# Kernel optimization log

Hardware: AMD Instinct MI355X
Metric: run time of the kernel (lower is better)

## Reference

```python
import jax, jax.numpy as jnp
import numpy as np

EPS = 1e-08


def setup_inputs() -> dict:
    key = jax.random.key(0)
    k_x, k_w1, k_b1, k_w2, k_b2 = jax.random.split(key, 5)
    B, C, T = 64, 64, 4000
    x = jax.random.normal(k_x, (B, C, T, 1), dtype=jnp.float32)
    # 1x1 Conv2D with in_channels=1, out_channels=8 -> weight is an 8-vector + bias
    w1 = jax.random.normal(k_w1, (8,), dtype=jnp.float32) * 0.5
    b1 = jax.random.normal(k_b1, (8,), dtype=jnp.float32) * 0.1
    w2 = jax.random.normal(k_w2, (8,), dtype=jnp.float32) * 0.5
    b2 = jax.random.normal(k_b2, (8,), dtype=jnp.float32) * 0.1
    # gamma is initialized to 0 in the module (residual identity at init);
    # use a nonzero value so the attention path is exercised numerically.
    gamma = jnp.float32(0.5)
    return {"x": x, "w1": w1, "b1": b1, "w2": w2, "b2": b2, "gamma": gamma}


def reference(x, w1, b1, w2, b2, gamma):
    B, C, T, _ = x.shape  # (B, num_ch, T, 1)
    # 1x1 conv with C_in=1: broadcast multiply-add, then flatten (T, 8) -> T*8
    q = (x * w1 + b1).reshape(B, C, T * 8)  # proj_query (B, C, T*8)
    k = (x * w2 + b2).reshape(B, C, T * 8)  # proj_key   (B, C, T*8)
    # energy = Q @ K^T  -> (B, C, C)
    energy = jnp.einsum('bcd,bed->bce', q, k)
    # custom min-max normalization along last axis, then softmax
    max_h = jnp.max(energy, axis=2, keepdims=True)
    min_h = jnp.min(energy, axis=2, keepdims=True)
    energy = (energy - min_h) / (max_h - min_h + EPS)
    attention = jax.nn.softmax(energy, axis=-1)
    xs = x[..., 0]  # squeeze last dim -> (B, C, T)
    # attention^T @ xs  (transpose_a=True)
    attended = jnp.einsum('bec,bet->bct', attention, xs)
    return gamma * attended[..., None] + x
```

## Files before the change

kernel.cpp:

```cpp
#include <hip/hip_runtime.h>

#define BB 64
#define CC 64
#define TT 4000

#define SLABS 16
#define TSLAB 250
#define GP_PITCH 264

#define TPB 128
#define NT2 ((TT + TPB - 1) / TPB)
#define XPITCH 132
#define APITCH 72

#define GPART_ELEMS ((size_t)SLABS * BB * CC * CC)
#define SPART_ELEMS ((size_t)SLABS * BB * CC)

typedef short short8 __attribute__((ext_vector_type(8)));
typedef float f32x16 __attribute__((ext_vector_type(16)));

__device__ __forceinline__ short f2bf(float f) {
    unsigned u = __float_as_uint(f);
    u = (u + 0x7FFFu + ((u >> 16) & 1u)) >> 16;
    return (short)u;
}
__device__ __forceinline__ float bfpair(unsigned u) {
    return __uint_as_float(u << 16) + __uint_as_float(u & 0xFFFF0000u);
}

__global__ __launch_bounds__(256)
void gram_mfma(const float* __restrict__ x, float* __restrict__ G_part,
               float* __restrict__ S_part) {
    __shared__ short xs[CC * GP_PITCH];
    __shared__ float sred[4 * 64];
    const int b    = blockIdx.x / SLABS;
    const int slab = blockIdx.x % SLABS;
    const int t0   = slab * TSLAB;
    const int tid  = threadIdx.x;
    const int lane = tid & 63;
    const int wave = tid >> 6;
    const float* xb = x + (size_t)b * CC * TT;

    for (int i = tid; i < 64 * 64; i += 256) {
        int row = i >> 6, tq = i & 63;
        float4 v = make_float4(0.f, 0.f, 0.f, 0.f);
        if (tq < 62) {
            v = *(const float4*)(xb + row * TT + t0 + 4 * tq);
        } else if (tq == 62) {
            const float* p = xb + row * TT + t0 + 248;
            v.x = p[0]; v.y = p[1];
        }
        short4 sv;
        sv.x = f2bf(v.x); sv.y = f2bf(v.y); sv.z = f2bf(v.z); sv.w = f2bf(v.w);
        int pc = (tq >> 1) ^ (row & 7);
        *(short4*)(xs + row * GP_PITCH + pc * 8 + (tq & 1) * 4) = sv;
    }
    __syncthreads();

    {
        const short* rowp = xs + lane * GP_PITCH;
        float s = 0.f;
        #pragma unroll
        for (int j = 0; j < 8; ++j) {
            int pc = (wave * 8 + j) ^ (lane & 7);
            uint2 u0 = *(const uint2*)(rowp + pc * 8);
            uint2 u1 = *(const uint2*)(rowp + pc * 8 + 4);
            s += bfpair(u0.x) + bfpair(u0.y) + bfpair(u1.x) + bfpair(u1.y);
        }
        sred[wave * 64 + lane] = s;
    }
    __syncthreads();
    if (tid < 64) {
        float s = sred[tid] + sred[64 + tid] + sred[128 + tid] + sred[192 + tid];
        S_part[(slab * BB + b) * CC + tid] = s;
    }

    const int r0 = (wave >> 1) * 32, c0 = (wave & 1) * 32;
    const int m = lane & 31, half = lane >> 5;
    f32x16 acc;
    #pragma unroll
    for (int z = 0; z < 16; ++z) acc[z] = 0.f;
    #pragma unroll
    for (int ks = 0; ks < 16; ++ks) {
        const int ck = ks * 2 + half;
        short8 av = *(const short8*)(xs + (r0 + m) * GP_PITCH + (ck ^ (m & 7)) * 8);
        short8 bv = *(const short8*)(xs + (c0 + m) * GP_PITCH + (ck ^ (m & 7)) * 8);
        acc = __builtin_amdgcn_mfma_f32_32x32x16_bf16(av, bv, acc, 0, 0, 0);
    }
    float* gp = G_part + ((size_t)slab * BB + b) * (CC * CC);
    #pragma unroll
    for (int r = 0; r < 16; ++r) {
        const int row = (r & 3) + 8 * (r >> 2) + 4 * half;
        gp[(r0 + row) * CC + (c0 + m)] = acc[r];
    }
}

__global__ __launch_bounds__(256)
void softmax_fused(const float* __restrict__ w1, const float* __restrict__ b1,
                   const float* __restrict__ w2, const float* __restrict__ b2,
                   const float* __restrict__ G_part, const float* __restrict__ S_part,
                   float* __restrict__ attG) {
    __shared__ float Es[64 * 65];
    __shared__ float Sb[64];
    __shared__ float red_mn[4 * 64], red_mx[4 * 64], red_sm[4 * 64];
    const int b   = blockIdx.x;
    const int tid = threadIdx.x;
    const int c = tid & 63, q = tid >> 6;

    for (int j = tid; j < 4096; j += 256) {
        float s = 0.f;
        #pragma unroll
        for (int sl = 0; sl < SLABS; ++sl)
            s += G_part[((size_t)sl * BB + b) * 4096 + j];
        Es[(j >> 6) * 65 + (j & 63)] = s;
    }
    if (tid < 64) {
        float s = 0.f;
        #pragma unroll
        for (int sl = 0; sl < SLABS; ++sl)
            s += S_part[(sl * BB + b) * CC + tid];
        Sb[tid] = s;
    }
    float A = 0.f, Bc = 0.f, Be = 0.f, Cc = 0.f;
    #pragma unroll
    for (int j = 0; j < 8; ++j) {
        float a1 = w1[j], a2 = w2[j], q1 = b1[j], q2 = b2[j];
        A += a1 * a2; Bc += a1 * q2; Be += q1 * a2; Cc += q1 * q2;
    }
    Cc *= (float)TT;
    __syncthreads();

    const float sc = Sb[c];
    float ev[16], mn = 1e30f, mx = -1e30f;
    #pragma unroll
    for (int i = 0; i < 16; ++i) {
        const int e = 16 * q + i;
        float en = A * Es[c * 65 + e] + Bc * sc + Be * Sb[e] + Cc;
        ev[i] = en;
        mn = fminf(mn, en); mx = fmaxf(mx, en);
    }
    red_mn[q * 64 + c] = mn; red_mx[q * 64 + c] = mx;
    __syncthreads();
    mn = fminf(fminf(red_mn[c], red_mn[64 + c]), fminf(red_mn[128 + c], red_mn[192 + c]));
    mx = fmaxf(fmaxf(red_mx[c], red_mx[64 + c]), fmaxf(red_mx[128 + c], red_mx[192 + c]));
    const float ninv = 1.f / (mx - mn + 1e-8f);
    float pv[16], ls = 0.f;
    #pragma unroll
    for (int i = 0; i < 16; ++i) {
        float p = __expf((ev[i] - mn) * ninv);
        pv[i] = p; ls += p;
    }
    red_sm[q * 64 + c] = ls;
    __syncthreads();
    const float rinv = 1.f / (red_sm[c] + red_sm[64 + c] + red_sm[128 + c] + red_sm[192 + c]);
    #pragma unroll
    for (int i = 0; i < 16; ++i) Es[c * 65 + 16 * q + i] = pv[i] * rinv;
    __syncthreads();
    float* ab = attG + (size_t)b * 4096;
    for (int j = tid; j < 4096; j += 256) {
        int cc = j >> 6, ee = j & 63;
        ab[j] = Es[ee * 65 + cc];
    }
}

__global__ __launch_bounds__(256)
void apply_mfma(const float* __restrict__ x, const float* __restrict__ attG,
                const float* __restrict__ gamma, float* __restrict__ out) {
    __shared__ float xs[CC * XPITCH];
    __shared__ short al[CC * APITCH];
    const int b  = blockIdx.x / NT2;
    const int t0 = (blockIdx.x % NT2) * TPB;
    const int tid = threadIdx.x;
    const int lane = tid & 63, wave = tid >> 6;
    const float* xb = x + (size_t)b * CC * TT;
    const float* ab = attG + (size_t)b * CC * CC;

    for (int i = tid; i < CC * (TPB / 4); i += 256) {
        int e = i >> 5, p = i & 31;
        int t = t0 + 4 * p;
        float4 v = make_float4(0.f, 0.f, 0.f, 0.f);
        if (t < TT) v = *(const float4*)(xb + e * TT + t);
        *(float4*)(xs + e * XPITCH + 4 * p) = v;
    }
    for (int i = tid; i < CC * CC / 4; i += 256) {
        int c = i >> 4, qq = i & 15;
        float4 v = *(const float4*)(ab + c * CC + 4 * qq);
        short4 sv;
        sv.x = f2bf(v.x); sv.y = f2bf(v.y); sv.z = f2bf(v.z); sv.w = f2bf(v.w);
        *(short4*)(al + c * APITCH + 4 * qq) = sv;
    }
    __syncthreads();

    const int m = lane & 31, half = lane >> 5;
    const int c0 = (wave & 1) * 32;
    const int tb = (wave >> 1) * 64;
    f32x16 acc0, acc1;
    #pragma unroll
    for (int z = 0; z < 16; ++z) { acc0[z] = 0.f; acc1[z] = 0.f; }

    #pragma unroll
    for (int ks = 0; ks < 4; ++ks) {
        short8 av = *(const short8*)(al + (c0 + m) * APITCH + ks * 16 + 8 * half);
        const int eb = ks * 16 + 8 * half;
        short8 bv0, bv1;
        #pragma unroll
        for (int j = 0; j < 8; ++j) {
            bv0[j] = f2bf(xs[(eb + j) * XPITCH + tb + m]);
            bv1[j] = f2bf(xs[(eb + j) * XPITCH + tb + 32 + m]);
        }
        acc0 = __builtin_amdgcn_mfma_f32_32x32x16_bf16(av, bv0, acc0, 0, 0, 0);
        acc1 = __builtin_amdgcn_mfma_f32_32x32x16_bf16(av, bv1, acc1, 0, 0, 0);
    }

    const float gm = gamma[0];
    float* ob = out + (size_t)b * CC * TT;
    #pragma unroll
    for (int r = 0; r < 16; ++r) {
        const int row = (r & 3) + 8 * (r >> 2) + 4 * half;
        const int c = c0 + row;
        const int tl0 = tb + m, tl1 = tb + 32 + m;
        const int tg0 = t0 + tl0, tg1 = t0 + tl1;
        if (tg0 < TT) ob[c * TT + tg0] = gm * acc0[r] + xs[c * XPITCH + tl0];
        if (tg1 < TT) ob[c * TT + tg1] = gm * acc1[r] + xs[c * XPITCH + tl1];
    }
}

extern "C" void kernel_launch(void* const* d_in, const int* in_sizes, int n_in,
                              void* d_out, int out_size, void* d_ws, size_t ws_size,
                              hipStream_t stream) {
    const float* x  = (const float*)d_in[0];
    const float* w1 = (const float*)d_in[1];
    const float* b1 = (const float*)d_in[2];
    const float* w2 = (const float*)d_in[3];
    const float* b2 = (const float*)d_in[4];
    const float* gm = (const float*)d_in[5];
    float* out = (float*)d_out;

    float* G_part = (float*)d_ws;
    float* S_part = G_part + GPART_ELEMS;
    float* attG   = S_part + SPART_ELEMS;

    hipLaunchKernelGGL(gram_mfma, dim3(BB * SLABS), dim3(256), 0, stream,
                       x, G_part, S_part);
    hipLaunchKernelGGL(softmax_fused, dim3(BB), dim3(256), 0, stream,
                       w1, b1, w2, b2, G_part, S_part, attG);
    hipLaunchKernelGGL(apply_mfma, dim3(BB * NT2), dim3(256), 0, stream,
                       x, attG, gm, out);
}
```

Before: 166.4 us.

## Halve gram slabs, batch loads, and pass attention as bf16 to apply kernel

The gram kernel now processes two 250-step chunks per block with 8 slabs instead of 16. This halves the partial Gram matrices written to and re-read from the workspace, and loads are batched eight float4s at a time for more memory-level parallelism. The softmax kernel reduces partials with float4 loads and writes the attention matrix directly as packed bf16, so the apply kernel loads it with wide short8 reads instead of converting per block. The trade-off is fewer gram blocks (512) and an extra barrier per chunk, which may reduce parallelism.

```diff
diff --git a/kernel.cpp b/kernel.cpp
--- a/kernel.cpp
+++ b/kernel.cpp
@@ -4,8 +4,9 @@
 #define CC 64
 #define TT 4000
 
-#define SLABS 16
+#define SLABS 8
 #define TSLAB 250
+#define SLABT (2 * TSLAB)
 #define GP_PITCH 264
 
 #define TPB 128
@@ -35,58 +36,78 @@
     __shared__ float sred[4 * 64];
     const int b    = blockIdx.x / SLABS;
     const int slab = blockIdx.x % SLABS;
-    const int t0   = slab * TSLAB;
     const int tid  = threadIdx.x;
     const int lane = tid & 63;
     const int wave = tid >> 6;
     const float* xb = x + (size_t)b * CC * TT;
 
-    for (int i = tid; i < 64 * 64; i += 256) {
-        int row = i >> 6, tq = i & 63;
-        float4 v = make_float4(0.f, 0.f, 0.f, 0.f);
-        if (tq < 62) {
-            v = *(const float4*)(xb + row * TT + t0 + 4 * tq);
-        } else if (tq == 62) {
-            const float* p = xb + row * TT + t0 + 248;
-            v.x = p[0]; v.y = p[1];
-        }
-        short4 sv;
-        sv.x = f2bf(v.x); sv.y = f2bf(v.y); sv.z = f2bf(v.z); sv.w = f2bf(v.w);
-        int pc = (tq >> 1) ^ (row & 7);
-        *(short4*)(xs + row * GP_PITCH + pc * 8 + (tq & 1) * 4) = sv;
-    }
-    __syncthreads();
-
-    {
-        const short* rowp = xs + lane * GP_PITCH;
-        float s = 0.f;
-        #pragma unroll
-        for (int j = 0; j < 8; ++j) {
-            int pc = (wave * 8 + j) ^ (lane & 7);
-            uint2 u0 = *(const uint2*)(rowp + pc * 8);
-            uint2 u1 = *(const uint2*)(rowp + pc * 8 + 4);
-            s += bfpair(u0.x) + bfpair(u0.y) + bfpair(u1.x) + bfpair(u1.y);
-        }
-        sred[wave * 64 + lane] = s;
-    }
+    const int r0 = (wave >> 1) * 32, c0 = (wave & 1) * 32;
+    const int m = lane & 31, half = lane >> 5;
+    f32x16 acc;
+    #pragma unroll
+    for (int z = 0; z < 16; ++z) acc[z] = 0.f;
+    float s_acc = 0.f;
+
+    for (int ch = 0; ch < 2; ++ch) {
+        const int t0 = slab * SLABT + ch * TSLAB;
+
+        #pragma unroll
+        for (int g = 0; g < 2; ++g) {
+            float4 v[8];
+            #pragma unroll
+            for (int k = 0; k < 8; ++k) {
+                const int i = tid + 256 * (g * 8 + k);
+                const int row = i >> 6, tq = i & 63;
+                float4 w = make_float4(0.f, 0.f, 0.f, 0.f);
+                if (tq < 62) {
+                    w = *(const float4*)(xb + row * TT + t0 + 4 * tq);
+                } else if (tq == 62) {
+                    const float* p = xb + row * TT + t0 + 248;
+                    w.x = p[0]; w.y = p[1];
+                }
+                v[k] = w;
+            }
+            #pragma unroll
+            for (int k = 0; k < 8; ++k) {
+                const int i = tid + 256 * (g * 8 + k);
+                const int row = i >> 6, tq = i & 63;
+                short4 sv;
+                sv.x = f2bf(v[k].x); sv.y = f2bf(v[k].y);
+                sv.z = f2bf(v[k].z); sv.w = f2bf(v[k].w);
+                const int pc = (tq >> 1) ^ (row & 7);
+                *(short4*)(xs + row * GP_PITCH + pc * 8 + (tq & 1) * 4) = sv;
+            }
+        }
+        __syncthreads();
+
+        {
+            const short* rowp = xs + lane * GP_PITCH;
+            #pragma unroll
+            for (int j = 0; j < 8; ++j) {
+                const int pc = (wave * 8 + j) ^ (lane & 7);
+                uint2 u0 = *(const uint2*)(rowp + pc * 8);
+                uint2 u1 = *(const uint2*)(rowp + pc * 8 + 4);
+                s_acc += bfpair(u0.x) + bfpair(u0.y) + bfpair(u1.x) + bfpair(u1.y);
+            }
+        }
+
+        #pragma unroll
+        for (int ks = 0; ks < 16; ++ks) {
+            const int ck = ks * 2 + half;
+            short8 av = *(const short8*)(xs + (r0 + m) * GP_PITCH + (ck ^ (m & 7)) * 8);
+            short8 bv = *(const short8*)(xs + (c0 + m) * GP_PITCH + (ck ^ (m & 7)) * 8);
+            acc = __builtin_amdgcn_mfma_f32_32x32x16_bf16(av, bv, acc, 0, 0, 0);
+        }
+        __syncthreads();
+    }
+
+    sred[wave * 64 + lane] = s_acc;
     __syncthreads();
     if (tid < 64) {
         float s = sred[tid] + sred[64 + tid] + sred[128 + tid] + sred[192 + tid];
         S_part[(slab * BB + b) * CC + tid] = s;
     }
 
-    const int r0 = (wave >> 1) * 32, c0 = (wave & 1) * 32;
-    const int m = lane & 31, half = lane >> 5;
-    f32x16 acc;
-    #pragma unroll
-    for (int z = 0; z < 16; ++z) acc[z] = 0.f;
-    #pragma unroll
-    for (int ks = 0; ks < 16; ++ks) {
-        const int ck = ks * 2 + half;
-        short8 av = *(const short8*)(xs + (r0 + m) * GP_PITCH + (ck ^ (m & 7)) * 8);
-        short8 bv = *(const short8*)(xs + (c0 + m) * GP_PITCH + (ck ^ (m & 7)) * 8);
-        acc = __builtin_amdgcn_mfma_f32_32x32x16_bf16(av, bv, acc, 0, 0, 0);
-    }
     float* gp = G_part + ((size_t)slab * BB + b) * (CC * CC);
     #pragma unroll
     for (int r = 0; r < 16; ++r) {
@@ -99,7 +120,7 @@
 void softmax_fused(const float* __restrict__ w1, const float* __restrict__ b1,
                    const float* __restrict__ w2, const float* __restrict__ b2,
                    const float* __restrict__ G_part, const float* __restrict__ S_part,
-                   float* __restrict__ attG) {
+                   unsigned short* __restrict__ attB) {
     __shared__ float Es[64 * 65];
     __shared__ float Sb[64];
     __shared__ float red_mn[4 * 64], red_mx[4 * 64], red_sm[4 * 64];
@@ -107,12 +128,18 @@
     const int tid = threadIdx.x;
     const int c = tid & 63, q = tid >> 6;
 
-    for (int j = tid; j < 4096; j += 256) {
-        float s = 0.f;
-        #pragma unroll
-        for (int sl = 0; sl < SLABS; ++sl)
-            s += G_part[((size_t)sl * BB + b) * 4096 + j];
-        Es[(j >> 6) * 65 + (j & 63)] = s;
+    #pragma unroll
+    for (int j4 = 0; j4 < 4; ++j4) {
+        const int jj = tid + 256 * j4;
+        float4 s = make_float4(0.f, 0.f, 0.f, 0.f);
+        #pragma unroll
+        for (int sl = 0; sl < SLABS; ++sl) {
+            const float4 g = *(const float4*)(G_part + ((size_t)sl * BB + b) * 4096 + 4 * jj);
+            s.x += g.x; s.y += g.y; s.z += g.z; s.w += g.w;
+        }
+        const int row = jj >> 4, col = (jj & 15) * 4;
+        float* e = Es + row * 65 + col;
+        e[0] = s.x; e[1] = s.y; e[2] = s.z; e[3] = s.w;
     }
     if (tid < 64) {
         float s = 0.f;
@@ -156,15 +183,18 @@
     #pragma unroll
     for (int i = 0; i < 16; ++i) Es[c * 65 + 16 * q + i] = pv[i] * rinv;
     __syncthreads();
-    float* ab = attG + (size_t)b * 4096;
-    for (int j = tid; j < 4096; j += 256) {
-        int cc = j >> 6, ee = j & 63;
-        ab[j] = Es[ee * 65 + cc];
+    unsigned short* ab = attB + (size_t)b * 4096;
+    #pragma unroll
+    for (int j2 = tid; j2 < 2048; j2 += 256) {
+        const int cc = j2 >> 5, e0 = (j2 & 31) * 2;
+        const unsigned lo = (unsigned short)f2bf(Es[e0 * 65 + cc]);
+        const unsigned hi = (unsigned short)f2bf(Es[(e0 + 1) * 65 + cc]);
+        *(unsigned*)(ab + cc * 64 + e0) = lo | (hi << 16);
     }
 }
 
 __global__ __launch_bounds__(256)
-void apply_mfma(const float* __restrict__ x, const float* __restrict__ attG,
+void apply_mfma(const float* __restrict__ x, const unsigned short* __restrict__ attB,
                 const float* __restrict__ gamma, float* __restrict__ out) {
     __shared__ float xs[CC * XPITCH];
     __shared__ short al[CC * APITCH];
@@ -173,21 +203,36 @@
     const int tid = threadIdx.x;
     const int lane = tid & 63, wave = tid >> 6;
     const float* xb = x + (size_t)b * CC * TT;
-    const float* ab = attG + (size_t)b * CC * CC;
-
-    for (int i = tid; i < CC * (TPB / 4); i += 256) {
-        int e = i >> 5, p = i & 31;
-        int t = t0 + 4 * p;
-        float4 v = make_float4(0.f, 0.f, 0.f, 0.f);
-        if (t < TT) v = *(const float4*)(xb + e * TT + t);
-        *(float4*)(xs + e * XPITCH + 4 * p) = v;
-    }
-    for (int i = tid; i < CC * CC / 4; i += 256) {
-        int c = i >> 4, qq = i & 15;
-        float4 v = *(const float4*)(ab + c * CC + 4 * qq);
-        short4 sv;
-        sv.x = f2bf(v.x); sv.y = f2bf(v.y); sv.z = f2bf(v.z); sv.w = f2bf(v.w);
-        *(short4*)(al + c * APITCH + 4 * qq) = sv;
+    const unsigned short* ab = attB + (size_t)b * 4096;
+
+    short8 avv[2];
+    #pragma unroll
+    for (int k = 0; k < 2; ++k)
+        avv[k] = *(const short8*)(ab + (tid + 256 * k) * 8);
+
+    #pragma unroll
+    for (int g = 0; g < 2; ++g) {
+        float4 v[4];
+        #pragma unroll
+        for (int k = 0; k < 4; ++k) {
+            const int i = tid + 256 * (g * 4 + k);
+            const int e = i >> 5, p = i & 31;
+            const int t = t0 + 4 * p;
+            v[k] = make_float4(0.f, 0.f, 0.f, 0.f);
+            if (t < TT) v[k] = *(const float4*)(xb + e * TT + t);
+        }
+        #pragma unroll
+        for (int k = 0; k < 4; ++k) {
+            const int i = tid + 256 * (g * 4 + k);
+            const int e = i >> 5, p = i & 31;
+            *(float4*)(xs + e * XPITCH + 4 * p) = v[k];
+        }
+    }
+    #pragma unroll
+    for (int k = 0; k < 2; ++k) {
+        const int i = tid + 256 * k;
+        const int cch = i >> 3, q8 = i & 7;
+        *(short8*)(al + cch * APITCH + q8 * 8) = avv[k];
     }
     __syncthreads();
 
@@ -238,12 +283,12 @@
 
     float* G_part = (float*)d_ws;
     float* S_part = G_part + GPART_ELEMS;
-    float* attG   = S_part + SPART_ELEMS;
+    unsigned short* attB = (unsigned short*)(S_part + SPART_ELEMS);
 
     hipLaunchKernelGGL(gram_mfma, dim3(BB * SLABS), dim3(256), 0, stream,
                        x, G_part, S_part);
     hipLaunchKernelGGL(softmax_fused, dim3(BB), dim3(256), 0, stream,
-                       w1, b1, w2, b2, G_part, S_part, attG);
+                       w1, b1, w2, b2, G_part, S_part, attB);
     hipLaunchKernelGGL(apply_mfma, dim3(BB * NT2), dim3(256), 0, stream,
-                       x, attG, gm, out);
-}
+                       x, attB, gm, out);
+}
```

New measurement: 156.3 us. 6.0% less time.
